# Kernel optimization log

Measured on AMD Instinct MI355X. Metric: run time of the kernel, lower is better.

The kernel has to match this reference:

```python
import math
import jax, jax.numpy as jnp
import numpy as np

S = 32.0
M1 = 1.0
M2 = 0.5
M3 = 0.0
MM = M2 * math.sin(math.pi - M2)
NUM_CLASSES = 100000
FEATURES = 512
BATCH = 512


def setup_inputs() -> dict:
    key = jax.random.key(0)
    k1, k2, k3 = jax.random.split(key, 3)
    inputs = jax.random.normal(k1, (BATCH, FEATURES), dtype=jnp.float32)
    labels = jax.random.randint(k2, (BATCH,), 0, NUM_CLASSES, dtype=jnp.int64)
    # xavier_uniform on [num_classes, features]
    limit = math.sqrt(6.0 / (NUM_CLASSES + FEATURES))
    weight = jax.random.uniform(k3, (NUM_CLASSES, FEATURES), minval=-limit, maxval=limit, dtype=jnp.float32)
    return {"inputs": inputs, "labels": labels, "weight": weight}


def reference(inputs, labels, weight):
    # L2 normalize (torch F.normalize uses eps=1e-12 clamp on norm)
    inp_n = inputs / jnp.maximum(jnp.linalg.norm(inputs, axis=1, keepdims=True), 1e-12)
    w_n = weight / jnp.maximum(jnp.linalg.norm(weight, axis=1, keepdims=True), 1e-12)
    cos_in = jnp.clip(inp_n @ w_n.T, -1.0 + 1e-6, 1.0 - 1e-6)  # [N, C]
    theta_in = jnp.arccos(cos_in)
    one_hot = jax.nn.one_hot(labels, NUM_CLASSES, dtype=cos_in.dtype)
    theta_out = theta_in + (theta_in * (M1 - 1.0) + M2) * one_hot
    cos_out = jnp.where(
        theta_out < math.pi,
        jnp.cos(theta_out) - M3 * one_hot,
        cos_in - MM * one_hot - M3 * one_hot,
    )
    outs = S * cos_out  # [N, C]
    # mean cross-entropy
    logp = jax.nn.log_softmax(outs, axis=1)
    n = jnp.arange(BATCH)
    loss = -jnp.mean(logp[n, labels])
    target_cos_in = cos_in[n, labels][:, None]
    target_theta_in = theta_in[n, labels][:, None]
    target_cos_out = cos_out[n, labels][:, None]
    return loss, outs, target_cos_in, target_theta_in, target_cos_out
```

## Files before the change

### kernel.cpp

```cpp
#include <hip/hip_runtime.h>
#include <stdint.h>

#define BATCH 512
#define FEAT 512
#define NCLS 100000
#define BM 128
#define BN 128
#define BK 64
#define NBLK_N 782
#define NCHUNK (NBLK_N * 2)
#define SCALE_S 32.0f
#define MARGIN 0.5f
#define MM_CONST 0.23971276930210156f
#define PI_F 3.14159265358979f

typedef unsigned int u32;
typedef unsigned short u16;
typedef __bf16 bf16x8 __attribute__((ext_vector_type(8)));
typedef float f32x4 __attribute__((ext_vector_type(4)));

__device__ __forceinline__ u16 f2bf(float f) {
  u32 u = __float_as_uint(f);
  u += 0x7fffu + ((u >> 16) & 1u);
  return (u16)(u >> 16);
}

__device__ __forceinline__ void async_copy16(const void* g, void* l) {
  __builtin_amdgcn_global_load_lds((const __attribute__((address_space(1))) u32*)g,
                                   (__attribute__((address_space(3))) u32*)l,
                                   16, 0, 0);
}

__device__ __forceinline__ float block_reduce_sum(float v, float* sbuf) {
  for (int off = 1; off < 64; off <<= 1) v += __shfl_xor(v, off, 64);
  int wid = threadIdx.x >> 6, lane = threadIdx.x & 63;
  __syncthreads();
  if (lane == 0) sbuf[wid] = v;
  __syncthreads();
  return sbuf[0] + sbuf[1] + sbuf[2] + sbuf[3];
}

__global__ __launch_bounds__(256) void norm_rows_kernel(const float* __restrict__ src,
                                                        u16* __restrict__ dst) {
  __shared__ float sbuf[4];
  int row = blockIdx.x;
  const float2* p = (const float2*)(src + (size_t)row * FEAT);
  float2 v = p[threadIdx.x];
  float ss = block_reduce_sum(v.x * v.x + v.y * v.y, sbuf);
  float inv = 1.0f / fmaxf(sqrtf(ss), 1e-12f);
  u16 a = f2bf(v.x * inv), b = f2bf(v.y * inv);
  ((u32*)(dst + (size_t)row * FEAT))[threadIdx.x] = (u32)a | ((u32)b << 16);
}

__global__ __launch_bounds__(256) void gemm_kernel(const u16* __restrict__ A,
                                                   const u16* __restrict__ B,
                                                   const int* __restrict__ labels,
                                                   float* __restrict__ outs,
                                                   float* __restrict__ partials) {
  __shared__ __align__(16) u16 sA[BM * BK];
  __shared__ __align__(16) u16 sB[BN * BK];
  __shared__ int sLab[BM];

  const int tid = threadIdx.x;
  const int lane = tid & 63;
  const int wid = tid >> 6;
  const int waveM = wid >> 1, waveN = wid & 1;
  const int bn = blockIdx.x, bm = blockIdx.y;
  const int quad = lane >> 4, l15 = lane & 15;

  if (tid < BM) sLab[tid] = labels[bm * BM + tid];

  int srow[4], scb[4];
#pragma unroll
  for (int rd = 0; rd < 4; ++rd) {
    int idx = rd * 256 + tid;
    int r = idx >> 3;
    srow[rd] = r;
    scb[rd] = (idx & 7) ^ (r & 7);
  }

  f32x4 acc[4][4] = {};

  for (int kt = 0; kt < FEAT / BK; ++kt) {
#pragma unroll
    for (int rd = 0; rd < 4; ++rd) {
      int r = srow[rd], cb = scb[rd];
      const u16* ga = A + (size_t)(bm * BM + r) * FEAT + kt * BK + cb * 8;
      int brow = bn * BN + r;
      if (brow >= NCLS) brow = NCLS - 1;
      const u16* gb = B + (size_t)brow * FEAT + kt * BK + cb * 8;
      int li = (rd * 256 + tid) * 8;
      async_copy16(ga, &sA[li]);
      async_copy16(gb, &sB[li]);
    }
    __syncthreads();
#pragma unroll
    for (int ks = 0; ks < 2; ++ks) {
      int j0 = ks * 4 + quad;
      bf16x8 aF[4], bF[4];
#pragma unroll
      for (int mi = 0; mi < 4; ++mi) {
        int r = waveM * 64 + mi * 16 + l15;
        aF[mi] = *(const bf16x8*)&sA[(r * 8 + (j0 ^ (r & 7))) * 8];
      }
#pragma unroll
      for (int ni = 0; ni < 4; ++ni) {
        int r = waveN * 64 + ni * 16 + l15;
        bF[ni] = *(const bf16x8*)&sB[(r * 8 + (j0 ^ (r & 7))) * 8];
      }
#pragma unroll
      for (int mi = 0; mi < 4; ++mi)
#pragma unroll
        for (int ni = 0; ni < 4; ++ni)
          acc[mi][ni] = __builtin_amdgcn_mfma_f32_16x16x32_bf16(aF[mi], bF[ni],
                                                                acc[mi][ni], 0, 0, 0);
    }
    __syncthreads();
  }

#pragma unroll
  for (int mi = 0; mi < 4; ++mi) {
#pragma unroll
    for (int reg = 0; reg < 4; ++reg) {
      int rloc = waveM * 64 + mi * 16 + quad * 4 + reg;
      int rg = bm * BM + rloc;
      int lab = sLab[rloc];
      float vals[4];
      float rmax = -1e30f;
#pragma unroll
      for (int ni = 0; ni < 4; ++ni) {
        int cg = bn * BN + waveN * 64 + ni * 16 + l15;
        float v = acc[mi][ni][reg];
        v = fminf(fmaxf(v, -1.0f + 1e-6f), 1.0f - 1e-6f);
        if (cg == lab) {
          float th = acosf(v) + MARGIN;
          v = (th < PI_F) ? cosf(th) : (v - MM_CONST);
        }
        v *= SCALE_S;
        if (cg < NCLS)
          outs[(size_t)rg * NCLS + cg] = v;
        else
          v = -1e30f;
        vals[ni] = v;
        rmax = fmaxf(rmax, v);
      }
#pragma unroll
      for (int off = 1; off < 16; off <<= 1) rmax = fmaxf(rmax, __shfl_xor(rmax, off, 64));
      float rsum = 0.f;
#pragma unroll
      for (int ni = 0; ni < 4; ++ni) rsum += __expf(vals[ni] - rmax);
#pragma unroll
      for (int off = 1; off < 16; off <<= 1) rsum += __shfl_xor(rsum, off, 64);
      if (l15 == 0) {
        float* p = partials + ((size_t)rg * NCHUNK + (bn * 2 + waveN)) * 2;
        p[0] = rmax;
        p[1] = rsum;
      }
    }
  }
}

__global__ __launch_bounds__(256) void combine_kernel(const float* __restrict__ partials,
                                                      const float* __restrict__ outs,
                                                      const int* __restrict__ labels,
                                                      float* __restrict__ loss_r) {
  int r = blockIdx.x, tid = threadIdx.x;
  const float* p = partials + (size_t)r * NCHUNK * 2;
  float m = -1e30f, l = 0.f;
  for (int i = tid; i < NCHUNK; i += 256) {
    float mi = p[2 * i], li = p[2 * i + 1];
    if (mi > m) { l = l * __expf(m - mi) + li; m = mi; }
    else l += li * __expf(mi - m);
  }
  for (int off = 1; off < 64; off <<= 1) {
    float mo = __shfl_xor(m, off, 64);
    float lo = __shfl_xor(l, off, 64);
    if (mo > m) { l = l * __expf(m - mo) + lo; m = mo; }
    else l += lo * __expf(mo - m);
  }
  __shared__ float sm[4], sl[4];
  int wv = tid >> 6, lane = tid & 63;
  if (lane == 0) { sm[wv] = m; sl[wv] = l; }
  __syncthreads();
  if (tid == 0) {
    for (int w = 1; w < 4; ++w) {
      float mo = sm[w], lo = sl[w];
      if (mo > m) { l = l * __expf(m - mo) + lo; m = mo; }
      else l += lo * __expf(mo - m);
    }
    float lse = m + logf(l);
    loss_r[r] = lse - outs[(size_t)r * NCLS + labels[r]];
  }
}

__global__ __launch_bounds__(256) void loss_kernel(const float* __restrict__ loss_r,
                                                   float* __restrict__ out0) {
  __shared__ float sbuf[4];
  float v = loss_r[threadIdx.x] + loss_r[threadIdx.x + 256];
  float s = block_reduce_sum(v, sbuf);
  if (threadIdx.x == 0) out0[0] = s * (1.0f / BATCH);
}

__global__ __launch_bounds__(256) void targets_kernel(const float* __restrict__ inputs,
                                                      const int* __restrict__ labels,
                                                      const float* __restrict__ weight,
                                                      float* __restrict__ tdst) {
  __shared__ float sbuf[4];
  int r = blockIdx.x, t = threadIdx.x;
  int lab = labels[r];
  const float2* px = (const float2*)(inputs + (size_t)r * FEAT);
  const float2* pw = (const float2*)(weight + (size_t)lab * FEAT);
  float2 x = px[t], w = pw[t];
  float dot = block_reduce_sum(x.x * w.x + x.y * w.y, sbuf);
  float sx = block_reduce_sum(x.x * x.x + x.y * x.y, sbuf);
  float sw = block_reduce_sum(w.x * w.x + w.y * w.y, sbuf);
  if (t == 0) {
    float inv = 1.0f / (fmaxf(sqrtf(sx), 1e-12f) * fmaxf(sqrtf(sw), 1e-12f));
    float ci = fminf(fmaxf(dot * inv, -1.0f + 1e-6f), 1.0f - 1e-6f);
    float th = acosf(ci);
    float t2 = th + MARGIN;
    float co = (t2 < PI_F) ? cosf(t2) : (ci - MM_CONST);
    tdst[r] = ci;
    tdst[BATCH + r] = th;
    tdst[2 * BATCH + r] = co;
  }
}

extern "C" void kernel_launch(void* const* d_in, const int* in_sizes, int n_in,
                              void* d_out, int out_size, void* d_ws, size_t ws_size,
                              hipStream_t stream) {
  const float* inputs = (const float*)d_in[0];
  const int* labels = (const int*)d_in[1];
  const float* weight = (const float*)d_in[2];
  float* out = (float*)d_out;
  float* outs = out + 1;
  float* tdst = out + 1 + (size_t)BATCH * NCLS;

  char* ws = (char*)d_ws;
  u16* wsA = (u16*)ws;
  u16* wsB = (u16*)(ws + 524288);
  float* partials = (float*)(ws + 524288 + 102400000);
  float* loss_r = (float*)(ws + 524288 + 102400000 + (size_t)BATCH * NCHUNK * 2 * 4);

  norm_rows_kernel<<<BATCH, 256, 0, stream>>>(inputs, wsA);
  norm_rows_kernel<<<NCLS, 256, 0, stream>>>(weight, wsB);
  gemm_kernel<<<dim3(NBLK_N, BATCH / BM), 256, 0, stream>>>(wsA, wsB, labels, outs, partials);
  combine_kernel<<<BATCH, 256, 0, stream>>>(partials, outs, labels, loss_r);
  loss_kernel<<<1, 256, 0, stream>>>(loss_r, out);
  targets_kernel<<<BATCH, 256, 0, stream>>>(inputs, labels, weight, tdst);
}
```

Before: 573.9 us.

## Normalize one row per wave and swap GEMM grid order for B-tile reuse

The row-normalization kernel now processes four rows per 256-thread block, one per wavefront, using float4 loads and a wave-only shuffle reduction instead of a block reduction with shared memory and syncthreads. The GEMM grid is transposed so the four M-blocks that share a weight tile are launched next to each other, which should improve L2 reuse of the normalized weight tiles. The label shared-memory staging is dropped in favour of direct global loads in the epilogue. The main goal is to cut launch and sync overhead in the 100k-row normalization and reduce weight re-reads from memory.

```diff
diff --git a/kernel.cpp b/kernel.cpp
--- a/kernel.cpp
+++ b/kernel.cpp
@@ -41,15 +41,24 @@
 }
 
 __global__ __launch_bounds__(256) void norm_rows_kernel(const float* __restrict__ src,
-                                                        u16* __restrict__ dst) {
-  __shared__ float sbuf[4];
-  int row = blockIdx.x;
-  const float2* p = (const float2*)(src + (size_t)row * FEAT);
-  float2 v = p[threadIdx.x];
-  float ss = block_reduce_sum(v.x * v.x + v.y * v.y, sbuf);
+                                                        u16* __restrict__ dst, int nrows) {
+  int row = (blockIdx.x << 2) + (threadIdx.x >> 6);
+  int lane = threadIdx.x & 63;
+  if (row >= nrows) return;
+  const float4* p = (const float4*)(src + (size_t)row * FEAT);
+  float4 a = p[lane], b = p[lane + 64];
+  float ss = a.x * a.x + a.y * a.y + a.z * a.z + a.w * a.w +
+             b.x * b.x + b.y * b.y + b.z * b.z + b.w * b.w;
+#pragma unroll
+  for (int off = 1; off < 64; off <<= 1) ss += __shfl_xor(ss, off, 64);
   float inv = 1.0f / fmaxf(sqrtf(ss), 1e-12f);
-  u16 a = f2bf(v.x * inv), b = f2bf(v.y * inv);
-  ((u32*)(dst + (size_t)row * FEAT))[threadIdx.x] = (u32)a | ((u32)b << 16);
+  u32 o0 = (u32)f2bf(a.x * inv) | ((u32)f2bf(a.y * inv) << 16);
+  u32 o1 = (u32)f2bf(a.z * inv) | ((u32)f2bf(a.w * inv) << 16);
+  u32 o2 = (u32)f2bf(b.x * inv) | ((u32)f2bf(b.y * inv) << 16);
+  u32 o3 = (u32)f2bf(b.z * inv) | ((u32)f2bf(b.w * inv) << 16);
+  uint2* d = (uint2*)(dst + (size_t)row * FEAT);
+  d[lane] = make_uint2(o0, o1);
+  d[lane + 64] = make_uint2(o2, o3);
 }
 
 __global__ __launch_bounds__(256) void gemm_kernel(const u16* __restrict__ A,
@@ -59,16 +68,13 @@
                                                    float* __restrict__ partials) {
   __shared__ __align__(16) u16 sA[BM * BK];
   __shared__ __align__(16) u16 sB[BN * BK];
-  __shared__ int sLab[BM];
 
   const int tid = threadIdx.x;
   const int lane = tid & 63;
   const int wid = tid >> 6;
   const int waveM = wid >> 1, waveN = wid & 1;
-  const int bn = blockIdx.x, bm = blockIdx.y;
+  const int bm = blockIdx.x, bn = blockIdx.y;
   const int quad = lane >> 4, l15 = lane & 15;
-
-  if (tid < BM) sLab[tid] = labels[bm * BM + tid];
 
   int srow[4], scb[4];
 #pragma unroll
@@ -124,7 +130,7 @@
     for (int reg = 0; reg < 4; ++reg) {
       int rloc = waveM * 64 + mi * 16 + quad * 4 + reg;
       int rg = bm * BM + rloc;
-      int lab = sLab[rloc];
+      int lab = labels[rg];
       float vals[4];
       float rmax = -1e30f;
 #pragma unroll
@@ -242,9 +248,9 @@
   float* partials = (float*)(ws + 524288 + 102400000);
   float* loss_r = (float*)(ws + 524288 + 102400000 + (size_t)BATCH * NCHUNK * 2 * 4);
 
-  norm_rows_kernel<<<BATCH, 256, 0, stream>>>(inputs, wsA);
-  norm_rows_kernel<<<NCLS, 256, 0, stream>>>(weight, wsB);
-  gemm_kernel<<<dim3(NBLK_N, BATCH / BM), 256, 0, stream>>>(wsA, wsB, labels, outs, partials);
+  norm_rows_kernel<<<BATCH / 4, 256, 0, stream>>>(inputs, wsA, BATCH);
+  norm_rows_kernel<<<(NCLS + 3) / 4, 256, 0, stream>>>(weight, wsB, NCLS);
+  gemm_kernel<<<dim3(BATCH / BM, NBLK_N), 256, 0, stream>>>(wsA, wsB, labels, outs, partials);
   combine_kernel<<<BATCH, 256, 0, stream>>>(partials, outs, labels, loss_r);
   loss_kernel<<<1, 256, 0, stream>>>(loss_r, out);
   targets_kernel<<<BATCH, 256, 0, stream>>>(inputs, labels, weight, tdst);
```

Result: no change. 577.3 us (+0.6%).
